# Optimization experiments

Hardware: AMD Instinct MI355X
Metric: run time of the kernel (lower is better)

Reference implementation:

```python
import jax, jax.numpy as jnp
import numpy as np

N, E, H, R = 16384, 262144, 256, 64
INV_SQRT_3 = 1.0 / np.sqrt(3.0)
INV_SQRT_H = 1.0 / np.sqrt(float(H))
INV_SQRT_2 = 1.0 / np.sqrt(2.0)


def ssilu(t):
    # ScaledSiLU: silu(x) / 0.6
    return jax.nn.silu(t) * (1.0 / 0.6)


def layernorm(x, g, b):
    m = jnp.mean(x, axis=-1, keepdims=True)
    v = jnp.var(x, axis=-1, keepdims=True)
    return (x - m) * jax.lax.rsqrt(v + 1e-5) * g + b


def gated_equivariant_block(x, v, Wv1, Wv2, Wu1, bu1, Wu2, bu2, out_ch):
    # x: [N, Cin], v: [N, 3, Cin]
    vec1 = jnp.linalg.norm(v @ Wv1, axis=-2)          # [N, Cin]
    vec2 = v @ Wv2                                     # [N, 3, out_ch]
    h = ssilu(jnp.concatenate([x, vec1], axis=-1) @ Wu1 + bu1) @ Wu2 + bu2
    xn, vn = h[..., :out_ch], h[..., out_ch:]
    return ssilu(xn), vn[:, None, :] * vec2


def setup_inputs() -> dict:
    key = jax.random.key(0)
    ks = iter(jax.random.split(key, 48))

    def w(shape, fan_in):
        return jax.random.normal(next(ks), shape, jnp.float32) / np.sqrt(float(fan_in))

    return {
        "x": jax.random.normal(next(ks), (N, H), jnp.float32),
        "vec": jax.random.normal(next(ks), (N, 3, H), jnp.float32),
        "edge_rbf": jax.random.uniform(next(ks), (E, R), jnp.float32),
        "edge_vector": jax.random.normal(next(ks), (E, 3), jnp.float32),
        # PaiNNMessage params
        "ln_g": jnp.ones((H,), jnp.float32), "ln_b": jnp.zeros((H,), jnp.float32),
        "W_x1": w((H, H), H), "b_x1": jnp.zeros((H,), jnp.float32),
        "W_x2": w((H, 3 * H), H), "b_x2": jnp.zeros((3 * H,), jnp.float32),
        "W_rbf": w((R, 3 * H), R), "b_rbf": jnp.zeros((3 * H,), jnp.float32),
        # PaiNNUpdate params
        "W_vp": w((H, 2 * H), H),
        "W_xv1": w((2 * H, H), 2 * H), "b_xv1": jnp.zeros((H,), jnp.float32),
        "W_xv2": w((H, 3 * H), H), "b_xv2": jnp.zeros((3 * H,), jnp.float32),
        # PaiNNOutput block 1 (H -> H//2)
        "o1_Wv1": w((H, H), H), "o1_Wv2": w((H, H // 2), H),
        "o1_Wu1": w((2 * H, H), 2 * H), "o1_bu1": jnp.zeros((H,), jnp.float32),
        "o1_Wu2": w((H, H), H), "o1_bu2": jnp.zeros((H,), jnp.float32),
        # PaiNNOutput block 2 (H//2 -> 1)
        "o2_Wv1": w((H // 2, H // 2), H // 2), "o2_Wv2": w((H // 2, 1), H // 2),
        "o2_Wu1": w((H, H // 2), H), "o2_bu1": jnp.zeros((H // 2,), jnp.float32),
        "o2_Wu2": w((H // 2, 2), H // 2), "o2_bu2": jnp.zeros((2,), jnp.float32),
        "edge_index": jax.random.randint(next(ks), (2, E), 0, N),
    }


def reference(x, vec, edge_rbf, edge_vector,
              ln_g, ln_b, W_x1, b_x1, W_x2, b_x2, W_rbf, b_rbf,
              W_vp, W_xv1, b_xv1, W_xv2, b_xv2,
              o1_Wv1, o1_Wv2, o1_Wu1, o1_bu1, o1_Wu2, o1_bu2,
              o2_Wv1, o2_Wv2, o2_Wu1, o2_bu1, o2_Wu2, o2_bu2,
              edge_index):
    src, dst = edge_index[0], edge_index[1]

    # ---- PaiNNMessage ----
    xh = ssilu(layernorm(x, ln_g, ln_b) @ W_x1 + b_x1) @ W_x2 + b_x2   # [N, 3H]
    rbfh = edge_rbf @ W_rbf + b_rbf                                     # [E, 3H]
    m = xh[src] * rbfh                                                  # gather + fuse
    m1, m2, m3 = m[:, :H], m[:, H:2 * H], m[:, 2 * H:]
    m2 = m2 * INV_SQRT_3
    vmsg = (vec[src] * m2[:, None, :] + m3[:, None, :] * edge_vector[:, :, None]) * INV_SQRT_H  # [E,3,H]
    dx = jax.ops.segment_sum(m1, dst, num_segments=N)
    dvec = jax.ops.segment_sum(vmsg, dst, num_segments=N)
    x = x + dx
    vec = vec + dvec

    # ---- PaiNNUpdate ----
    vp = vec @ W_vp                                    # [N, 3, 2H]
    vec1, vec2 = vp[..., :H], vp[..., H:]
    vec_dot = jnp.sum(vec1 * vec2, axis=1) * INV_SQRT_H            # [N, H]
    vnorm = jnp.sqrt(jnp.sum(vec2 * vec2, axis=-2) + 1e-8)          # [N, H]
    xvh = ssilu(jnp.concatenate([x, vnorm], axis=-1) @ W_xv1 + b_xv1) @ W_xv2 + b_xv2
    xv1, xv2, xv3 = xvh[:, :H], xvh[:, H:2 * H], xvh[:, 2 * H:]
    x = x + (xv1 + xv2 * vec_dot) * INV_SQRT_2
    vec = vec + xv3[:, None, :] * vec1

    # ---- PaiNNOutput ----
    x, vec = gated_equivariant_block(x, vec, o1_Wv1, o1_Wv2, o1_Wu1, o1_bu1, o1_Wu2, o1_bu2, H // 2)
    x, vec = gated_equivariant_block(x, vec, o2_Wv1, o2_Wv2, o2_Wu1, o2_bu1, o2_Wu2, o2_bu2, 1)
    return jnp.squeeze(vec, axis=-1)   # [N, 3]
```

## Files before the change

### kernel.cpp

```cpp
#include <hip/hip_runtime.h>
#include <math.h>

#define NN 16384
#define EE 262144
#define HH 256

#define INV_SQRT_3f 0.57735026918962576f
#define INV_SQRT_Hf 0.0625f
#define INV_SQRT_2f 0.70710678118654752f
#define SSILU_SCALE 1.6666666666666667f

typedef __attribute__((ext_vector_type(8))) short bf16x8;
typedef __attribute__((ext_vector_type(4))) float f32x4;

__device__ __forceinline__ float ssilu_f(float v) {
    return v * (1.0f / (1.0f + __expf(-v))) * SSILU_SCALE;
}
__device__ __forceinline__ float b2f(short s) {
    unsigned int u = ((unsigned int)(unsigned short)s) << 16;
    return __uint_as_float(u);
}
__device__ __forceinline__ short f2b(float f) {
    unsigned int u = __float_as_uint(f);
    unsigned int r = (u + 0x7fff + ((u >> 16) & 1)) >> 16;
    return (short)r;
}

__global__ void __launch_bounds__(256) ln_kernel(const float* __restrict__ x,
                                                 const float* __restrict__ g,
                                                 const float* __restrict__ b,
                                                 short* __restrict__ oh,
                                                 short* __restrict__ ol) {
    int n = blockIdx.x;
    int t = threadIdx.x;
    float v = x[(long)n * HH + t];
    float s = v, s2 = v * v;
    #pragma unroll
    for (int off = 32; off > 0; off >>= 1) {
        s  += __shfl_down(s, off);
        s2 += __shfl_down(s2, off);
    }
    __shared__ float red[8];
    int wave = t >> 6, lane = t & 63;
    if (lane == 0) { red[wave] = s; red[4 + wave] = s2; }
    __syncthreads();
    __shared__ float mr[2];
    if (t == 0) {
        float ts = red[0] + red[1] + red[2] + red[3];
        float ts2 = red[4] + red[5] + red[6] + red[7];
        float mean = ts * (1.0f / HH);
        float var = ts2 * (1.0f / HH) - mean * mean;
        mr[0] = mean;
        mr[1] = rsqrtf(var + 1e-5f);
    }
    __syncthreads();
    float o = (v - mr[0]) * mr[1] * g[t] + b[t];
    short hh = f2b(o);
    oh[(long)n * HH + t] = hh;
    ol[(long)n * HH + t] = f2b(o - b2f(hh));
}

struct WtArgs {
    const float* W[12];
    int K[12];
    int N[12];
    int off[13];
};

__global__ void __launch_bounds__(256) wt_split_all(WtArgs a,
                                                    short* __restrict__ WTh,
                                                    short* __restrict__ WTl) {
    int idx = blockIdx.x * 256 + threadIdx.x;
    int s = 0;
    #pragma unroll
    for (int i = 1; i < 12; i++) s += (idx >= a.off[i]) ? 1 : 0;
    int local = idx - a.off[s];
    int K = a.K[s], N = a.N[s];
    int k = local / N, n = local - k * N;
    float w = a.W[s][local];
    short hh = f2b(w);
    long o = (long)a.off[s] + (long)n * K + k;
    WTh[o] = hh;
    WTl[o] = f2b(w - b2f(hh));
}

__global__ void __launch_bounds__(256) split4_kernel(const float* __restrict__ in,
                                                     short* __restrict__ h,
                                                     short* __restrict__ l) {
    long i = ((long)blockIdx.x * 256 + threadIdx.x) * 4;
    float4 v = *(const float4*)(in + i);
    short4 oh, ol;
    oh.x = f2b(v.x); ol.x = f2b(v.x - b2f(oh.x));
    oh.y = f2b(v.y); ol.y = f2b(v.y - b2f(oh.y));
    oh.z = f2b(v.z); ol.z = f2b(v.z - b2f(oh.z));
    oh.w = f2b(v.w); ol.w = f2b(v.w - b2f(oh.w));
    *(short4*)(h + i) = oh;
    *(short4*)(l + i) = ol;
}

__global__ void __launch_bounds__(256) mfma_gemm(const short* __restrict__ Ah,
                                                 const short* __restrict__ Al,
                                                 const short* __restrict__ Wh,
                                                 const short* __restrict__ Wl,
                                                 const float* __restrict__ bias,
                                                 void* __restrict__ Ch,
                                                 short* __restrict__ Cl,
                                                 int M, int K, int N, int act) {
    int tid = threadIdx.x;
    int wave = tid >> 6, lane = tid & 63;
    int quad = lane >> 4, l16 = lane & 15;
    long bm = (long)blockIdx.x * 128 + wave * 32;
    long bn = (long)blockIdx.y * 64;
    long a0 = (bm + l16) * K + quad * 8;
    long a1 = a0 + (long)16 * K;
    long w0 = (bn + l16) * K + quad * 8;

    f32x4 acc[2][4];
    #pragma unroll
    for (int f = 0; f < 2; f++)
        #pragma unroll
        for (int t = 0; t < 4; t++) acc[f][t] = (f32x4){0.f, 0.f, 0.f, 0.f};

    bf16x8 cah[2], cal[2], cbh[4], cbl[4];
    cah[0] = *(const bf16x8*)(Ah + a0);
    cah[1] = *(const bf16x8*)(Ah + a1);
    cal[0] = *(const bf16x8*)(Al + a0);
    cal[1] = *(const bf16x8*)(Al + a1);
    #pragma unroll
    for (int t = 0; t < 4; t++) {
        long wo = w0 + (long)t * 16 * K;
        cbh[t] = *(const bf16x8*)(Wh + wo);
        cbl[t] = *(const bf16x8*)(Wl + wo);
    }

    for (int k0 = 0; k0 < K; k0 += 32) {
        int k1 = k0 + 32;
        bf16x8 nah[2], nal[2], nbh[4], nbl[4];
        if (k1 < K) {
            nah[0] = *(const bf16x8*)(Ah + a0 + k1);
            nah[1] = *(const bf16x8*)(Ah + a1 + k1);
            nal[0] = *(const bf16x8*)(Al + a0 + k1);
            nal[1] = *(const bf16x8*)(Al + a1 + k1);
            #pragma unroll
            for (int t = 0; t < 4; t++) {
                long wo = w0 + (long)t * 16 * K + k1;
                nbh[t] = *(const bf16x8*)(Wh + wo);
                nbl[t] = *(const bf16x8*)(Wl + wo);
            }
        }
        #pragma unroll
        for (int t = 0; t < 4; t++) {
            #pragma unroll
            for (int f = 0; f < 2; f++) {
                acc[f][t] = __builtin_amdgcn_mfma_f32_16x16x32_bf16(cah[f], cbh[t], acc[f][t], 0, 0, 0);
                acc[f][t] = __builtin_amdgcn_mfma_f32_16x16x32_bf16(cal[f], cbh[t], acc[f][t], 0, 0, 0);
                acc[f][t] = __builtin_amdgcn_mfma_f32_16x16x32_bf16(cah[f], cbl[t], acc[f][t], 0, 0, 0);
            }
        }
        if (k1 < K) {
            cah[0] = nah[0]; cah[1] = nah[1];
            cal[0] = nal[0]; cal[1] = nal[1];
            #pragma unroll
            for (int t = 0; t < 4; t++) { cbh[t] = nbh[t]; cbl[t] = nbl[t]; }
        }
    }

    #pragma unroll
    for (int f = 0; f < 2; f++) {
        long row0 = bm + f * 16 + quad * 4;
        #pragma unroll
        for (int t = 0; t < 4; t++) {
            long col = bn + t * 16 + l16;
            float bv = bias ? bias[col] : 0.f;
            #pragma unroll
            for (int r = 0; r < 4; r++) {
                float v = acc[f][t][r] + bv;
                if (act & 1) v = ssilu_f(v);
                long idx = (row0 + r) * N + col;
                if (Cl) {
                    short hh = f2b(v);
                    ((short*)Ch)[idx] = hh;
                    Cl[idx] = f2b(v - b2f(hh));
                } else if (act & 2) {
                    ((short*)Ch)[idx] = f2b(v);
                } else {
                    ((float*)Ch)[idx] = v;
                }
            }
        }
    }
}

__global__ void __launch_bounds__(256) zero_kernel(int* __restrict__ p, int n) {
    int i = blockIdx.x * 256 + threadIdx.x;
    if (i < n) p[i] = 0;
}

__global__ void __launch_bounds__(256) hist_kernel(const int* __restrict__ eidx,
                                                   int* __restrict__ cnt) {
    int e = blockIdx.x * 256 + threadIdx.x;
    atomicAdd(&cnt[eidx[EE + e]], 1);
}

__global__ void __launch_bounds__(256) scan_kernel(int* __restrict__ cursor,
                                                   int* __restrict__ rowptr) {
    int t = threadIdx.x;
    int base_i = t * 64;
    int tsum = 0;
    for (int i = 0; i < 64; i++) tsum += cursor[base_i + i];
    __shared__ int ls[256];
    ls[t] = tsum;
    __syncthreads();
    for (int off = 1; off < 256; off <<= 1) {
        int v = (t >= off) ? ls[t - off] : 0;
        __syncthreads();
        ls[t] += v;
        __syncthreads();
    }
    int running = ls[t] - tsum;
    for (int i = 0; i < 64; i++) {
        int c = cursor[base_i + i];
        rowptr[base_i + i] = running;
        cursor[base_i + i] = running;
        running += c;
    }
    if (t == 255) rowptr[NN] = running;
}

__global__ void __launch_bounds__(256) scatter_kernel(const int* __restrict__ eidx,
                                                      const float* __restrict__ ev,
                                                      int* __restrict__ cursor,
                                                      int* __restrict__ perm,
                                                      int* __restrict__ dsts,
                                                      int* __restrict__ srcs,
                                                      float* __restrict__ evs) {
    int e = blockIdx.x * 256 + threadIdx.x;
    int s_ = eidx[e];
    int d_ = eidx[EE + e];
    int pos = atomicAdd(&cursor[d_], 1);
    perm[pos] = e;
    dsts[pos] = d_;
    srcs[pos] = s_;
    evs[pos * 3 + 0] = ev[e * 3 + 0];
    evs[pos * 3 + 1] = ev[e * 3 + 1];
    evs[pos * 3 + 2] = ev[e * 3 + 2];
}

__global__ void __launch_bounds__(256) edge_gather_kernel(
        const float* __restrict__ rbf,
        const short* __restrict__ Wrh,
        const short* __restrict__ Wrl,
        const float* __restrict__ b_rbf,
        const float* __restrict__ xh,
        const float* __restrict__ vec,
        const int* __restrict__ perm,
        const int* __restrict__ dsts,
        const int* __restrict__ srcs,
        const float* __restrict__ evs,
        float* __restrict__ x1,
        float* __restrict__ vecacc) {
    int tid = threadIdx.x;
    int wave = tid >> 6, lane = tid & 63;
    int quad = lane >> 4, l16 = lane & 15;
    int bm = blockIdx.x * 128;
    int base = wave * 32;

    __shared__ __align__(16) float mlds[128][66];
    __shared__ int dst_s[128], src_s[128];
    __shared__ float ev_s[128][3];

    if (lane < 32) {
        int i = base + lane;
        dst_s[i] = dsts[bm + i];
        src_s[i] = srcs[bm + i];
        ev_s[i][0] = evs[(long)(bm + i) * 3 + 0];
        ev_s[i][1] = evs[(long)(bm + i) * 3 + 1];
        ev_s[i][2] = evs[(long)(bm + i) * 3 + 2];
    }

    int r0 = bm + wave * 32 + l16;
    int e0 = perm[r0];
    int e1 = perm[r0 + 16];
    bf16x8 afh[2][2], afl[2][2];
    #pragma unroll
    for (int f = 0; f < 2; f++) {
        long ebase = (long)(f == 0 ? e0 : e1) * 64 + quad * 8;
        #pragma unroll
        for (int ks = 0; ks < 2; ks++) {
            float4 ua = *(const float4*)(rbf + ebase + ks * 32);
            float4 ub = *(const float4*)(rbf + ebase + ks * 32 + 4);
            float vv[8] = {ua.x, ua.y, ua.z, ua.w, ub.x, ub.y, ub.z, ub.w};
            bf16x8 hh, ll;
            #pragma unroll
            for (int j = 0; j < 8; j++) {
                short hb = f2b(vv[j]);
                hh[j] = hb;
                ll[j] = f2b(vv[j] - b2f(hb));
            }
            afh[f][ks] = hh;
            afl[f][ks] = ll;
        }
    }

    for (int sec = 0; sec < 3; sec++) {
        for (int tile = 0; tile < 4; tile++) {
            int bn = sec * 256 + tile * 64;
            f32x4 acc[2][4];
            #pragma unroll
            for (int t = 0; t < 4; t++) {
                float bv = b_rbf[bn + t * 16 + l16];
                acc[0][t] = (f32x4){bv, bv, bv, bv};
                acc[1][t] = (f32x4){bv, bv, bv, bv};
            }
            #pragma unroll
            for (int t = 0; t < 4; t++) {
                #pragma unroll
                for (int ks = 0; ks < 2; ks++) {
                    long wo = (long)(bn + t * 16 + l16) * 64 + ks * 32 + quad * 8;
                    bf16x8 bh = *(const bf16x8*)(Wrh + wo);
                    bf16x8 bl = *(const bf16x8*)(Wrl + wo);
                    #pragma unroll
                    for (int f = 0; f < 2; f++) {
                        acc[f][t] = __builtin_amdgcn_mfma_f32_16x16x32_bf16(afh[f][ks], bh, acc[f][t], 0, 0, 0);
                        acc[f][t] = __builtin_amdgcn_mfma_f32_16x16x32_bf16(afl[f][ks], bh, acc[f][t], 0, 0, 0);
                        acc[f][t] = __builtin_amdgcn_mfma_f32_16x16x32_bf16(afh[f][ks], bl, acc[f][t], 0, 0, 0);
                    }
                }
            }
            #pragma unroll
            for (int f = 0; f < 2; f++)
                #pragma unroll
                for (int t = 0; t < 4; t++)
                    #pragma unroll
                    for (int r = 0; r < 4; r++)
                        mlds[base + f * 16 + quad * 4 + r][t * 16 + l16] = acc[f][t][r];

            int colx = tile * 64 + lane;
            if (sec == 0) {
                float a = 0.f;
                int dprev = dst_s[base];
                #pragma unroll 4
                for (int i = 0; i < 32; i++) {
                    int d = dst_s[base + i];
                    if (d != dprev) {
                        atomicAdd(&x1[(long)dprev * 256 + colx], a);
                        a = 0.f;
                        dprev = d;
                    }
                    long xb = (long)src_s[base + i] * 768;
                    a += mlds[base + i][lane] * xh[xb + colx];
                }
                atomicAdd(&x1[(long)dprev * 256 + colx], a);
            } else if (sec == 1) {
                float a0 = 0.f, a1 = 0.f, a2 = 0.f;
                int dprev = dst_s[base];
                #pragma unroll 4
                for (int i = 0; i < 32; i++) {
                    int d = dst_s[base + i];
                    if (d != dprev) {
                        long vb = (long)dprev * 768 + colx;
                        atomicAdd(&vecacc[vb], a0);
                        atomicAdd(&vecacc[vb + 256], a1);
                        atomicAdd(&vecacc[vb + 512], a2);
                        a0 = a1 = a2 = 0.f;
                        dprev = d;
                    }
                    long xb = (long)src_s[base + i] * 768;
                    float m2 = mlds[base + i][lane] * (INV_SQRT_3f * INV_SQRT_Hf) *
                               xh[xb + 256 + colx];
                    a0 += vec[xb + colx] * m2;
                    a1 += vec[xb + 256 + colx] * m2;
                    a2 += vec[xb + 512 + colx] * m2;
                }
                long vb = (long)dprev * 768 + colx;
                atomicAdd(&vecacc[vb], a0);
                atomicAdd(&vecacc[vb + 256], a1);
                atomicAdd(&vecacc[vb + 512], a2);
            } else {
                float a0 = 0.f, a1 = 0.f, a2 = 0.f;
                int dprev = dst_s[base];
                #pragma unroll 4
                for (int i = 0; i < 32; i++) {
                    int d = dst_s[base + i];
                    if (d != dprev) {
                        long vb = (long)dprev * 768 + colx;
                        atomicAdd(&vecacc[vb], a0);
                        atomicAdd(&vecacc[vb + 256], a1);
                        atomicAdd(&vecacc[vb + 512], a2);
                        a0 = a1 = a2 = 0.f;
                        dprev = d;
                    }
                    long xb = (long)src_s[base + i] * 768;
                    float m3 = mlds[base + i][lane] * INV_SQRT_Hf * xh[xb + 512 + colx];
                    a0 += m3 * ev_s[base + i][0];
                    a1 += m3 * ev_s[base + i][1];
                    a2 += m3 * ev_s[base + i][2];
                }
                long vb = (long)dprev * 768 + colx;
                atomicAdd(&vecacc[vb], a0);
                atomicAdd(&vecacc[vb + 256], a1);
                atomicAdd(&vecacc[vb + 512], a2);
            }
        }
    }
}

__global__ void __launch_bounds__(256) vdot_cat_kernel(const float* __restrict__ vec1,
                                                       const short* __restrict__ vec2,
                                                       const float* __restrict__ x1,
                                                       float* __restrict__ vdot,
                                                       short* __restrict__ cath,
                                                       short* __restrict__ catl) {
    int idx = blockIdx.x * 256 + threadIdx.x;
    int n = idx >> 8, h = idx & 255;
    float dsum = 0.f, s2 = 0.f;
    #pragma unroll
    for (int d = 0; d < 3; d++) {
        long r = (long)(n * 3 + d) * 256 + h;
        float a = vec1[r];
        float b = b2f(vec2[r]);
        dsum += a * b;
        s2 += b * b;
    }
    vdot[idx] = dsum * INV_SQRT_Hf;
    float xv = x1[idx];
    short hh = f2b(xv);
    cath[(long)n * 512 + h] = hh;
    catl[(long)n * 512 + h] = f2b(xv - b2f(hh));
    float vn = sqrtf(s2 + 1e-8f);
    short vh = f2b(vn);
    cath[(long)n * 512 + 256 + h] = vh;
    catl[(long)n * 512 + 256 + h] = f2b(vn - b2f(vh));
}

__global__ void __launch_bounds__(256) e4_kernel(float* __restrict__ x1,
                                                 float* __restrict__ vecacc,
                                                 const float* __restrict__ vec1,
                                                 const float* __restrict__ vdot,
                                                 const short* __restrict__ xvh_h,
                                                 const short* __restrict__ xvh_l) {
    int idx = blockIdx.x * 256 + threadIdx.x;
    int n = idx >> 8, h = idx & 255;
    long b0 = (long)n * 768 + h;
    float xv1 = b2f(xvh_h[b0])       + b2f(xvh_l[b0]);
    float xv2 = b2f(xvh_h[b0 + 256]) + b2f(xvh_l[b0 + 256]);
    float xv3 = b2f(xvh_h[b0 + 512]) + b2f(xvh_l[b0 + 512]);
    x1[idx] = x1[idx] + (xv1 + xv2 * vdot[idx]) * INV_SQRT_2f;
    #pragma unroll
    for (int d = 0; d < 3; d++) {
        long r = (long)(n * 3 + d) * 256 + h;
        vecacc[r] = vecacc[r] + xv3 * vec1[r];
    }
}

__global__ void __launch_bounds__(256) normcat_kernel(const float* __restrict__ xin,
                                                      const short* __restrict__ w,
                                                      short* __restrict__ cath,
                                                      short* __restrict__ catl,
                                                      int Cx, int C, int shift) {
    int idx = blockIdx.x * 256 + threadIdx.x;
    int cols = 1 << shift;
    int n = idx >> shift, c = idx & (cols - 1);
    float v;
    if (c < Cx) {
        v = xin[(long)n * Cx + c];
    } else {
        int cc = c - Cx;
        float s = 0.f;
        #pragma unroll
        for (int d = 0; d < 3; d++) {
            float a = b2f(w[(long)(n * 3 + d) * C + cc]);
            s += a * a;
        }
        v = sqrtf(s);
    }
    short hh = f2b(v);
    cath[idx] = hh;
    catl[idx] = f2b(v - b2f(hh));
}

__global__ void __launch_bounds__(256) gate1_kernel(const float* __restrict__ h1,
                                                    const short* __restrict__ w2h,
                                                    const short* __restrict__ w2l,
                                                    float* __restrict__ x3,
                                                    short* __restrict__ vecCh,
                                                    short* __restrict__ vecCl) {
    int idx = blockIdx.x * 256 + threadIdx.x;
    int n = idx >> 7, c = idx & 127;
    x3[idx] = ssilu_f(h1[(long)n * 256 + c]);
    float vn = h1[(long)n * 256 + 128 + c];
    #pragma unroll
    for (int d = 0; d < 3; d++) {
        long r = (long)(n * 3 + d) * 128 + c;
        float wv = b2f(w2h[r]) + b2f(w2l[r]);
        float v = vn * wv;
        short hh = f2b(v);
        vecCh[r] = hh;
        vecCl[r] = f2b(v - b2f(hh));
    }
}

__global__ void __launch_bounds__(256) g12_kernel(const short* __restrict__ vecCh,
                                                  const short* __restrict__ vecCl,
                                                  const float* __restrict__ Wv2,
                                                  float* __restrict__ w4) {
    int row = blockIdx.x * 4 + (threadIdx.x >> 6);
    int lane = threadIdx.x & 63;
    long r0 = (long)row * 128 + lane;
    float v0 = b2f(vecCh[r0]) + b2f(vecCl[r0]);
    float v1 = b2f(vecCh[r0 + 64]) + b2f(vecCl[r0 + 64]);
    float s = v0 * Wv2[lane] + v1 * Wv2[64 + lane];
    #pragma unroll
    for (int off = 32; off > 0; off >>= 1) s += __shfl_down(s, off);
    if (lane == 0) w4[row] = s;
}

__global__ void __launch_bounds__(256) final_kernel(const float* __restrict__ t5,
                                                    const float* __restrict__ Wu2,
                                                    const float* __restrict__ bu2,
                                                    const float* __restrict__ w4,
                                                    float* __restrict__ out) {
    int n = blockIdx.x * 4 + (threadIdx.x >> 6);
    int lane = threadIdx.x & 63;
    float s = t5[(long)n * 128 + lane] * Wu2[lane * 2 + 1] +
              t5[(long)n * 128 + 64 + lane] * Wu2[(64 + lane) * 2 + 1];
    #pragma unroll
    for (int off = 32; off > 0; off >>= 1) s += __shfl_down(s, off);
    float val = __shfl(s, 0) + bu2[1];
    if (lane < 3) out[(long)n * 3 + lane] = val * w4[(long)n * 3 + lane];
}

extern "C" void kernel_launch(void* const* d_in, const int* in_sizes, int n_in,
                              void* d_out, int out_size, void* d_ws, size_t ws_size,
                              hipStream_t stream) {
    const float* x          = (const float*)d_in[0];
    const float* vec        = (const float*)d_in[1];
    const float* edge_rbf   = (const float*)d_in[2];
    const float* edge_vector= (const float*)d_in[3];
    const float* ln_g       = (const float*)d_in[4];
    const float* ln_b       = (const float*)d_in[5];
    const float* W_x1       = (const float*)d_in[6];
    const float* b_x1       = (const float*)d_in[7];
    const float* W_x2       = (const float*)d_in[8];
    const float* b_x2       = (const float*)d_in[9];
    const float* W_rbf      = (const float*)d_in[10];
    const float* b_rbf      = (const float*)d_in[11];
    const float* W_vp       = (const float*)d_in[12];
    const float* W_xv1      = (const float*)d_in[13];
    const float* b_xv1      = (const float*)d_in[14];
    const float* W_xv2      = (const float*)d_in[15];
    const float* b_xv2      = (const float*)d_in[16];
    const float* o1_Wv1     = (const float*)d_in[17];
    const float* o1_Wv2     = (const float*)d_in[18];
    const float* o1_Wu1     = (const float*)d_in[19];
    const float* o1_bu1     = (const float*)d_in[20];
    const float* o1_Wu2     = (const float*)d_in[21];
    const float* o1_bu2     = (const float*)d_in[22];
    const float* o2_Wv1     = (const float*)d_in[23];
    const float* o2_Wv2     = (const float*)d_in[24];
    const float* o2_Wu1     = (const float*)d_in[25];
    const float* o2_bu1     = (const float*)d_in[26];
    const float* o2_Wu2     = (const float*)d_in[27];
    const float* o2_bu2     = (const float*)d_in[28];
    const int*   edge_index = (const int*)d_in[29];
    float* out = (float*)d_out;
    float* ws  = (float*)d_ws;

    const size_t S = (size_t)NN * 256;
    const size_t Q = S / 4;
    float* x1      = ws;
    float* vecacc  = ws + 4 * Q;
    short* wtb     = (short*)(ws + 16 * Q);
    const long WLO = 1114112;
    short* xln_h = (short*)(ws + 18 * Q);
    short* xln_l = (short*)(ws + 20 * Q);
    short* t1_h  = (short*)(ws + 22 * Q);
    short* t1_l  = (short*)(ws + 24 * Q);
    float* xh    = ws + 30 * Q;
    int* rowptr    = (int*)(ws + 48 * Q);
    int* cursor    = rowptr + (NN + 1);
    int* perm      = cursor + NN;
    int* dsts      = perm + EE;
    int* srcs      = dsts + EE;
    float* evs     = (float*)(srcs + EE);
    short* vah   = (short*)(ws + 18 * Q);
    short* val_  = (short*)(ws + 24 * Q);
    float* vec1  = ws + 30 * Q;
    short* vec2b = (short*)(ws + 42 * Q);
    float* vdot  = ws + 48 * Q;
    short* catb_h = (short*)(ws + 18 * Q);
    short* catb_l = (short*)(ws + 22 * Q);
    short* t2_h  = (short*)(ws + 26 * Q);
    short* t2_l  = (short*)(ws + 28 * Q);
    short* xvh_h = (short*)(ws + 18 * Q);
    short* xvh_l = (short*)(ws + 42 * Q);
    short* vah2  = (short*)(ws + 18 * Q);
    short* val2  = (short*)(ws + 24 * Q);
    short* w1b   = (short*)(ws + 30 * Q);
    short* w2_h  = (short*)(ws + 36 * Q);
    short* w2_l  = (short*)(ws + 39 * Q);
    short* cat2_h = (short*)(ws + 42 * Q);
    short* cat2_l = (short*)(ws + 46 * Q);
    short* t4_h  = (short*)(ws + 18 * Q);
    short* t4_l  = (short*)(ws + 20 * Q);
    float* h1    = ws + 22 * Q;
    float* x3    = ws + 26 * Q;
    short* vecC_h = (short*)(ws + 28 * Q);
    short* vecC_l = (short*)(ws + 31 * Q);
    short* w3b   = (short*)(ws + 34 * Q);
    float* w4    = ws + 37 * Q;
    short* cat3_h = (short*)(ws + 38 * Q);
    short* cat3_l = (short*)(ws + 40 * Q);
    float* t5    = ws + 42 * Q;

    short* WT_x1    = wtb;
    short* WT_x2    = wtb + 65536;
    short* WT_vp    = wtb + 262144;
    short* WT_xv1   = wtb + 393216;
    short* WT_xv2   = wtb + 524288;
    short* WT_o1Wv1 = wtb + 720896;
    short* WT_o1Wv2 = wtb + 786432;
    short* WT_o1Wu1 = wtb + 819200;
    short* WT_o1Wu2 = wtb + 950272;
    short* WT_o2Wv1 = wtb + 1015808;
    short* WT_o2Wu1 = wtb + 1032192;
    short* WT_rbf   = wtb + 1064960;

    WtArgs wa;
    const float* wsrc[12] = {W_x1, W_x2, W_vp, W_xv1, W_xv2, o1_Wv1, o1_Wv2,
                             o1_Wu1, o1_Wu2, o2_Wv1, o2_Wu1, W_rbf};
    int wk[12] = {256, 256, 256, 512, 256, 256, 256, 512, 256, 128, 256, 64};
    int wn[12] = {256, 768, 512, 256, 768, 256, 128, 256, 256, 128, 128, 768};
    int off = 0;
    for (int i = 0; i < 12; i++) {
        wa.W[i] = wsrc[i]; wa.K[i] = wk[i]; wa.N[i] = wn[i];
        wa.off[i] = off; off += wk[i] * wn[i];
    }
    wa.off[12] = off;
    wt_split_all<<<off / 256, 256, 0, stream>>>(wa, wtb, wtb + WLO);

    hipMemcpyAsync(x1, x, S * sizeof(float), hipMemcpyDeviceToDevice, stream);
    hipMemcpyAsync(vecacc, vec, 3 * S * sizeof(float), hipMemcpyDeviceToDevice, stream);

    ln_kernel<<<NN, 256, 0, stream>>>(x, ln_g, ln_b, xln_h, xln_l);
    mfma_gemm<<<dim3(NN / 128, 4), 256, 0, stream>>>(xln_h, xln_l, WT_x1, WT_x1 + WLO,
                                                     b_x1, t1_h, t1_l, NN, 256, 256, 1);
    mfma_gemm<<<dim3(NN / 128, 12), 256, 0, stream>>>(t1_h, t1_l, WT_x2, WT_x2 + WLO,
                                                      b_x2, xh, nullptr, NN, 256, 768, 0);

    zero_kernel<<<(NN + 255) / 256, 256, 0, stream>>>(cursor, NN);
    hist_kernel<<<EE / 256, 256, 0, stream>>>(edge_index, cursor);
    scan_kernel<<<1, 256, 0, stream>>>(cursor, rowptr);
    scatter_kernel<<<EE / 256, 256, 0, stream>>>(edge_index, edge_vector, cursor,
                                                 perm, dsts, srcs, evs);
    edge_gather_kernel<<<EE / 128, 256, 0, stream>>>(
        edge_rbf, WT_rbf, WT_rbf + WLO, b_rbf, xh, vec,
        perm, dsts, srcs, evs, x1, vecacc);
    split4_kernel<<<3 * S / 1024, 256, 0, stream>>>(vecacc, vah, val_);

    mfma_gemm<<<dim3(3 * NN / 128, 4), 256, 0, stream>>>(vah, val_, WT_vp, WT_vp + WLO,
                                                         nullptr, vec1, nullptr,
                                                         3 * NN, 256, 256, 0);
    mfma_gemm<<<dim3(3 * NN / 128, 4), 256, 0, stream>>>(vah, val_, WT_vp + 65536,
                                                         WT_vp + WLO + 65536,
                                                         nullptr, vec2b, nullptr,
                                                         3 * NN, 256, 256, 2);
    vdot_cat_kernel<<<NN, 256, 0, stream>>>(vec1, vec2b, x1, vdot, catb_h, catb_l);
    mfma_gemm<<<dim3(NN / 128, 4), 256, 0, stream>>>(catb_h, catb_l, WT_xv1, WT_xv1 + WLO,
                                                     b_xv1, t2_h, t2_l, NN, 512, 256, 1);
    mfma_gemm<<<dim3(NN / 128, 12), 256, 0, stream>>>(t2_h, t2_l, WT_xv2, WT_xv2 + WLO,
                                                      b_xv2, xvh_h, xvh_l, NN, 256, 768, 0);
    e4_kernel<<<NN, 256, 0, stream>>>(x1, vecacc, vec1, vdot, xvh_h, xvh_l);

    split4_kernel<<<3 * S / 1024, 256, 0, stream>>>(vecacc, vah2, val2);
    mfma_gemm<<<dim3(3 * NN / 128, 4), 256, 0, stream>>>(vah2, val2, WT_o1Wv1, WT_o1Wv1 + WLO,
                                                         nullptr, w1b, nullptr,
                                                         3 * NN, 256, 256, 2);
    mfma_gemm<<<dim3(3 * NN / 128, 2), 256, 0, stream>>>(vah2, val2, WT_o1Wv2, WT_o1Wv2 + WLO,
                                                         nullptr, w2_h, w2_l,
                                                         3 * NN, 256, 128, 0);
    normcat_kernel<<<NN * 512 / 256, 256, 0, stream>>>(x1, w1b, cat2_h, cat2_l, 256, 256, 9);
    mfma_gemm<<<dim3(NN / 128, 4), 256, 0, stream>>>(cat2_h, cat2_l, WT_o1Wu1, WT_o1Wu1 + WLO,
                                                     o1_bu1, t4_h, t4_l, NN, 512, 256, 1);
    mfma_gemm<<<dim3(NN / 128, 4), 256, 0, stream>>>(t4_h, t4_l, WT_o1Wu2, WT_o1Wu2 + WLO,
                                                     o1_bu2, h1, nullptr, NN, 256, 256, 0);
    gate1_kernel<<<NN * 128 / 256, 256, 0, stream>>>(h1, w2_h, w2_l, x3, vecC_h, vecC_l);

    mfma_gemm<<<dim3(3 * NN / 128, 2), 256, 0, stream>>>(vecC_h, vecC_l, WT_o2Wv1,
                                                         WT_o2Wv1 + WLO, nullptr,
                                                         w3b, nullptr, 3 * NN, 128, 128, 2);
    g12_kernel<<<3 * NN / 4, 256, 0, stream>>>(vecC_h, vecC_l, o2_Wv2, w4);
    normcat_kernel<<<NN * 256 / 256, 256, 0, stream>>>(x3, w3b, cat3_h, cat3_l, 128, 128, 8);
    mfma_gemm<<<dim3(NN / 128, 2), 256, 0, stream>>>(cat3_h, cat3_l, WT_o2Wu1, WT_o2Wu1 + WLO,
                                                     o2_bu1, t5, nullptr, NN, 256, 128, 1);
    final_kernel<<<NN / 4, 256, 0, stream>>>(t5, o2_Wu2, o2_bu2, w4, out);
}
```

Baseline: 1.579 ms.

## Split edge gather over eight waves of 16 edges and fold x copy into layernorm

The edge gather kernel now launches 512 threads per 128-edge block, so each wave handles 16 edges instead of 32. This halves per-wave register use (accumulators and A fragments) and the serial segment-sum loop length, aiming for more waves in flight to hide gather latency. The cost is that each wave reloads the same W_rbf fragments, so those loads double per block, and per-wave atomic flushes may rise. Separately, the device-to-device copy of x into the x1 accumulator is removed and the layernorm kernel writes x1 while it reads x, saving one memory pass.

```diff
diff --git a/kernel.cpp b/kernel.cpp
--- a/kernel.cpp
+++ b/kernel.cpp
@@ -30,10 +30,12 @@
                                                  const float* __restrict__ g,
                                                  const float* __restrict__ b,
                                                  short* __restrict__ oh,
-                                                 short* __restrict__ ol) {
+                                                 short* __restrict__ ol,
+                                                 float* __restrict__ x1) {
     int n = blockIdx.x;
     int t = threadIdx.x;
     float v = x[(long)n * HH + t];
+    x1[(long)n * HH + t] = v;
     float s = v, s2 = v * v;
     #pragma unroll
     for (int off = 32; off > 0; off >>= 1) {
@@ -246,7 +248,7 @@
     evs[pos * 3 + 2] = ev[e * 3 + 2];
 }
 
-__global__ void __launch_bounds__(256) edge_gather_kernel(
+__global__ void __launch_bounds__(512, 8) edge_gather_kernel(
         const float* __restrict__ rbf,
         const short* __restrict__ Wrh,
         const short* __restrict__ Wrl,
@@ -263,13 +265,13 @@
     int wave = tid >> 6, lane = tid & 63;
     int quad = lane >> 4, l16 = lane & 15;
     int bm = blockIdx.x * 128;
-    int base = wave * 32;
+    int base = wave * 16;
 
     __shared__ __align__(16) float mlds[128][66];
     __shared__ int dst_s[128], src_s[128];
     __shared__ float ev_s[128][3];
 
-    if (lane < 32) {
+    if (lane < 16) {
         int i = base + lane;
         dst_s[i] = dsts[bm + i];
         src_s[i] = srcs[bm + i];
@@ -278,13 +280,10 @@
         ev_s[i][2] = evs[(long)(bm + i) * 3 + 2];
     }
 
-    int r0 = bm + wave * 32 + l16;
-    int e0 = perm[r0];
-    int e1 = perm[r0 + 16];
-    bf16x8 afh[2][2], afl[2][2];
-    #pragma unroll
-    for (int f = 0; f < 2; f++) {
-        long ebase = (long)(f == 0 ? e0 : e1) * 64 + quad * 8;
+    int e0 = perm[bm + base + l16];
+    bf16x8 afh[2], afl[2];
+    {
+        long ebase = (long)e0 * 64 + quad * 8;
         #pragma unroll
         for (int ks = 0; ks < 2; ks++) {
             float4 ua = *(const float4*)(rbf + ebase + ks * 32);
@@ -297,50 +296,41 @@
                 hh[j] = hb;
                 ll[j] = f2b(vv[j] - b2f(hb));
             }
-            afh[f][ks] = hh;
-            afl[f][ks] = ll;
+            afh[ks] = hh;
+            afl[ks] = ll;
         }
     }
 
     for (int sec = 0; sec < 3; sec++) {
         for (int tile = 0; tile < 4; tile++) {
             int bn = sec * 256 + tile * 64;
-            f32x4 acc[2][4];
+            f32x4 acc[4];
             #pragma unroll
             for (int t = 0; t < 4; t++) {
                 float bv = b_rbf[bn + t * 16 + l16];
-                acc[0][t] = (f32x4){bv, bv, bv, bv};
-                acc[1][t] = (f32x4){bv, bv, bv, bv};
-            }
-            #pragma unroll
-            for (int t = 0; t < 4; t++) {
+                acc[t] = (f32x4){bv, bv, bv, bv};
                 #pragma unroll
                 for (int ks = 0; ks < 2; ks++) {
                     long wo = (long)(bn + t * 16 + l16) * 64 + ks * 32 + quad * 8;
                     bf16x8 bh = *(const bf16x8*)(Wrh + wo);
                     bf16x8 bl = *(const bf16x8*)(Wrl + wo);
-                    #pragma unroll
-                    for (int f = 0; f < 2; f++) {
-                        acc[f][t] = __builtin_amdgcn_mfma_f32_16x16x32_bf16(afh[f][ks], bh, acc[f][t], 0, 0, 0);
-                        acc[f][t] = __builtin_amdgcn_mfma_f32_16x16x32_bf16(afl[f][ks], bh, acc[f][t], 0, 0, 0);
-                        acc[f][t] = __builtin_amdgcn_mfma_f32_16x16x32_bf16(afh[f][ks], bl, acc[f][t], 0, 0, 0);
-                    }
+                    acc[t] = __builtin_amdgcn_mfma_f32_16x16x32_bf16(afh[ks], bh, acc[t], 0, 0, 0);
+                    acc[t] = __builtin_amdgcn_mfma_f32_16x16x32_bf16(afl[ks], bh, acc[t], 0, 0, 0);
+                    acc[t] = __builtin_amdgcn_mfma_f32_16x16x32_bf16(afh[ks], bl, acc[t], 0, 0, 0);
                 }
             }
             #pragma unroll
-            for (int f = 0; f < 2; f++)
+            for (int t = 0; t < 4; t++)
                 #pragma unroll
-                for (int t = 0; t < 4; t++)
-                    #pragma unroll
-                    for (int r = 0; r < 4; r++)
-                        mlds[base + f * 16 + quad * 4 + r][t * 16 + l16] = acc[f][t][r];
+                for (int r = 0; r < 4; r++)
+                    mlds[base + quad * 4 + r][t * 16 + l16] = acc[t][r];
 
             int colx = tile * 64 + lane;
             if (sec == 0) {
                 float a = 0.f;
                 int dprev = dst_s[base];
                 #pragma unroll 4
-                for (int i = 0; i < 32; i++) {
+                for (int i = 0; i < 16; i++) {
                     int d = dst_s[base + i];
                     if (d != dprev) {
                         atomicAdd(&x1[(long)dprev * 256 + colx], a);
@@ -355,7 +345,7 @@
                 float a0 = 0.f, a1 = 0.f, a2 = 0.f;
                 int dprev = dst_s[base];
                 #pragma unroll 4
-                for (int i = 0; i < 32; i++) {
+                for (int i = 0; i < 16; i++) {
                     int d = dst_s[base + i];
                     if (d != dprev) {
                         long vb = (long)dprev * 768 + colx;
@@ -380,7 +370,7 @@
                 float a0 = 0.f, a1 = 0.f, a2 = 0.f;
                 int dprev = dst_s[base];
                 #pragma unroll 4
-                for (int i = 0; i < 32; i++) {
+                for (int i = 0; i < 16; i++) {
                     int d = dst_s[base + i];
                     if (d != dprev) {
                         long vb = (long)dprev * 768 + colx;
@@ -639,10 +629,9 @@
     wa.off[12] = off;
     wt_split_all<<<off / 256, 256, 0, stream>>>(wa, wtb, wtb + WLO);
 
-    hipMemcpyAsync(x1, x, S * sizeof(float), hipMemcpyDeviceToDevice, stream);
     hipMemcpyAsync(vecacc, vec, 3 * S * sizeof(float), hipMemcpyDeviceToDevice, stream);
 
-    ln_kernel<<<NN, 256, 0, stream>>>(x, ln_g, ln_b, xln_h, xln_l);
+    ln_kernel<<<NN, 256, 0, stream>>>(x, ln_g, ln_b, xln_h, xln_l, x1);
     mfma_gemm<<<dim3(NN / 128, 4), 256, 0, stream>>>(xln_h, xln_l, WT_x1, WT_x1 + WLO,
                                                      b_x1, t1_h, t1_l, NN, 256, 256, 1);
     mfma_gemm<<<dim3(NN / 128, 12), 256, 0, stream>>>(t1_h, t1_l, WT_x2, WT_x2 + WLO,
@@ -653,7 +642,7 @@
     scan_kernel<<<1, 256, 0, stream>>>(cursor, rowptr);
     scatter_kernel<<<EE / 256, 256, 0, stream>>>(edge_index, edge_vector, cursor,
                                                  perm, dsts, srcs, evs);
-    edge_gather_kernel<<<EE / 128, 256, 0, stream>>>(
+    edge_gather_kernel<<<EE / 128, 512, 0, stream>>>(
         edge_rbf, WT_rbf, WT_rbf + WLO, b_rbf, xh, vec,
         perm, dsts, srcs, evs, x1, vecacc);
     split4_kernel<<<3 * S / 1024, 256, 0, stream>>>(vecacc, vah, val_);
```

New measurement: 1.479 ms. 1.07x faster.
